# Kernel tuning notes

Measured on AMD Instinct MI355X. Metric: run time of the kernel, lower is better.

The kernel has to match this reference:

```python
import jax, jax.numpy as jnp
import numpy as np

B, S, H, I, E, K = 1, 2048, 1024, 512, 16, 4


def setup_inputs() -> dict:
    key = jax.random.key(0)
    k0, k1, k2, k3, k4, k5 = jax.random.split(key, 6)
    hidden_states = jax.random.normal(k0, (B, S, H), jnp.float32)
    T = B * S
    topk_idx = jax.random.randint(k1, (T, K), 0, E, dtype=jnp.int32)
    raw = jax.random.uniform(k2, (T, K), jnp.float32)
    topk_weight = raw / jnp.sum(raw, axis=-1, keepdims=True)  # normalized top-k gate weights
    scale = 0.02
    w_gate = jax.random.normal(k3, (E, H, I), jnp.float32) * scale
    w_up = jax.random.normal(k4, (E, H, I), jnp.float32) * scale
    w_down = jax.random.normal(k5, (E, I, H), jnp.float32) * scale
    return {
        "hidden_states": hidden_states,
        "topk_idx": topk_idx,
        "topk_weight": topk_weight,
        "w_gate": w_gate,
        "w_up": w_up,
        "w_down": w_down,
    }


def reference(hidden_states, topk_idx, topk_weight, w_gate, w_up, w_down):
    # hidden_states: [B,S,H]; topk_idx/topk_weight: [T,K]; w_*: [E,H,I]/[E,I,H]
    b, s, h = hidden_states.shape
    t = b * s
    e = w_gate.shape[0]
    x = hidden_states.reshape(t, h)
    # routing_weights.scatter_(1, topk_idx, topk_weight)
    routing_weights = jnp.zeros((t, e), x.dtype).at[
        jnp.arange(t)[:, None], topk_idx
    ].set(topk_weight)
    # per-expert gated MLP over all tokens (math identical to masked dispatch:
    # tokens with routing weight 0 contribute nothing)
    g = jnp.einsum("th,ehi->eti", x, w_gate)  # [E,T,I]
    u = jnp.einsum("th,ehi->eti", x, w_up)
    d = jnp.einsum("eti,eih->eth", jax.nn.silu(g) * u, w_down)  # [E,T,H]
    out = jnp.einsum("eth,te->th", d, routing_weights)  # weighted combine
    return out.reshape(b, s, h)
```

## Files before the change

### kernel.cpp

```cpp
#include <hip/hip_runtime.h>
#include <hip/hip_bf16.h>
#include <stdint.h>

#define HH 1024
#define II 512
#define EE 16
#define TT 2048
#define KTOP 4
#define PP (TT * KTOP)
#define MAXROWS 12288

typedef unsigned short u16;
typedef unsigned int u32;
typedef __attribute__((ext_vector_type(8))) short short8;
typedef __attribute__((ext_vector_type(4))) float f32x4;
typedef __attribute__((ext_vector_type(4))) unsigned short u16x4;
typedef __attribute__((ext_vector_type(8))) unsigned short u16x8;
typedef __attribute__((ext_vector_type(4))) unsigned int u32x4;

__device__ __forceinline__ u16 f2bf(float f) {
  union { float f; unsigned u; } v; v.f = f;
  unsigned r = v.u + 0x7fffu + ((v.u >> 16) & 1u);
  return (u16)(r >> 16);
}
__device__ __forceinline__ float bf2f(u16 b) {
  union { unsigned u; float f; } v; v.u = ((unsigned)b) << 16; return v.f;
}

__device__ __forceinline__ void gld16(const u16* g, u16* l) {
  __builtin_amdgcn_global_load_lds(
      (const __attribute__((address_space(1))) unsigned int*)g,
      (__attribute__((address_space(3))) unsigned int*)l, 16, 0, 0);
}

union PLds {
  int s_e[PP];
  u32 t32[128][68];
};

__global__ __launch_bounds__(1024) void prep_fused(
    const float* __restrict__ x, const int* __restrict__ tidx,
    const float* __restrict__ tw,
    const float* __restrict__ wg, const float* __restrict__ wu,
    const float* __restrict__ wd,
    u16* __restrict__ xb, u16* __restrict__ WgT, u16* __restrict__ WuT,
    u16* __restrict__ WdT,
    int* __restrict__ perm, float* __restrict__ wt, int* __restrict__ rowof,
    int* __restrict__ tile_e, int* __restrict__ tile_r,
    int* __restrict__ ntiles) {
  __shared__ PLds L;
  __shared__ int whist[16][16];
  __shared__ int wbase[16][16];
  __shared__ int pad_lo[EE], pad_hi[EE];

  const int bid = blockIdx.x;
  const int tid = threadIdx.x;

  if (bid == 0) {
    const int lane = tid & 63;
    const int wv = tid >> 6;

#pragma unroll
    for (int i = 0; i < 2; i++) {
      const int t = tid + i * 1024;
      const int4 v = ((const int4*)tidx)[t];
      const bool v0 = (v.x != v.y) && (v.x != v.z) && (v.x != v.w);
      const bool v1 = (v.y != v.z) && (v.y != v.w);
      const bool v2 = (v.z != v.w);
      L.s_e[t * 4 + 0] = v.x | (v0 ? 16 : 0);
      L.s_e[t * 4 + 1] = v.y | (v1 ? 16 : 0);
      L.s_e[t * 4 + 2] = v.z | (v2 ? 16 : 0);
      L.s_e[t * 4 + 3] = v.w | 16;
    }
    __syncthreads();

    int h0, h1, h2, h3, h4, h5, h6, h7, h8, h9, h10, h11, h12, h13, h14, h15;
    h0=h1=h2=h3=h4=h5=h6=h7=h8=h9=h10=h11=h12=h13=h14=h15=0;
    const unsigned long long ltm = (1ull << lane) - 1ull;
    for (int c = 0; c < 8; c++) {
      const int p = (wv << 9) + (c << 6) + lane;
      const int se = L.s_e[p];
      const int e = se & 15;
      const bool valid = (se & 16) != 0;
      int rank = 0;
#define RANK_STEP(J, HJ)                                            \
      {                                                             \
        unsigned long long m = __ballot(valid && (e == J));         \
        if (valid && (e == J)) rank = HJ + __popcll(m & ltm);       \
        HJ += __popcll(m);                                          \
      }
      RANK_STEP(0, h0)  RANK_STEP(1, h1)  RANK_STEP(2, h2)  RANK_STEP(3, h3)
      RANK_STEP(4, h4)  RANK_STEP(5, h5)  RANK_STEP(6, h6)  RANK_STEP(7, h7)
      RANK_STEP(8, h8)  RANK_STEP(9, h9)  RANK_STEP(10, h10) RANK_STEP(11, h11)
      RANK_STEP(12, h12) RANK_STEP(13, h13) RANK_STEP(14, h14) RANK_STEP(15, h15)
#undef RANK_STEP
      if (valid) L.s_e[p] = se | (rank << 16);
    }
    if (lane == 0) {
      whist[wv][0] = h0;   whist[wv][1] = h1;   whist[wv][2] = h2;   whist[wv][3] = h3;
      whist[wv][4] = h4;   whist[wv][5] = h5;   whist[wv][6] = h6;   whist[wv][7] = h7;
      whist[wv][8] = h8;   whist[wv][9] = h9;   whist[wv][10] = h10; whist[wv][11] = h11;
      whist[wv][12] = h12; whist[wv][13] = h13; whist[wv][14] = h14; whist[wv][15] = h15;
    }
    __syncthreads();

    if (tid == 0) {
      int off = 0, nt = 0;
      for (int j = 0; j < EE; j++) {
        int tot = 0;
        for (int w = 0; w < 16; w++) { wbase[w][j] = off + tot; tot += whist[w][j]; }
        const int cap = (tot + 127) & ~127;
        pad_lo[j] = off + tot;
        pad_hi[j] = off + cap;
        for (int m0 = 0; m0 < cap; m0 += 128) { tile_e[nt] = j; tile_r[nt] = off + m0; nt++; }
        off += cap;
      }
      *ntiles = nt;
    }
    __syncthreads();

#pragma unroll
    for (int i = 0; i < 8; i++) {
      const int p = i * 1024 + tid;
      const int se = L.s_e[p];
      int pos = -1;
      if (se & 16) {
        const int e = se & 15;
        const int r = se >> 16;
        pos = wbase[p >> 9][e] + r;
        perm[pos] = p >> 2;
        wt[pos] = tw[p];
      }
      rowof[p] = pos;
    }
    for (int j = 0; j < EE; j++) {
      const int lo = pad_lo[j], hi = pad_hi[j];
      for (int i = lo + tid; i < hi; i += 1024) {
        perm[i] = 0;
        wt[i] = 0.f;
      }
    }
    return;
  }

  if (bid <= 128) {
    const int base = ((bid - 1) * 1024 + tid) * 16;
    f32x4 v0 = *(const f32x4*)(x + base);
    f32x4 v1 = *(const f32x4*)(x + base + 4);
    f32x4 v2 = *(const f32x4*)(x + base + 8);
    f32x4 v3 = *(const f32x4*)(x + base + 12);
    u16x8 o0 = { f2bf(v0[0]), f2bf(v0[1]), f2bf(v0[2]), f2bf(v0[3]),
                 f2bf(v1[0]), f2bf(v1[1]), f2bf(v1[2]), f2bf(v1[3]) };
    u16x8 o1 = { f2bf(v2[0]), f2bf(v2[1]), f2bf(v2[2]), f2bf(v2[3]),
                 f2bf(v3[0]), f2bf(v3[1]), f2bf(v3[2]), f2bf(v3[3]) };
    *(u16x8*)(xb + base) = o0;
    *(u16x8*)(xb + base + 8) = o1;
    return;
  }

  const int pb = bid - 129;
  const int matsel = pb >> 9;
  const int within = pb & 511;
  const int zz = within >> 5;
  const int sub = within & 31;
  const float* src; u16* dst; int R, C, xi, yi;
  if (matsel == 0)      { src = wg; dst = WgT; R = HH; C = II; xi = sub & 3; yi = sub >> 2; }
  else if (matsel == 1) { src = wu; dst = WuT; R = HH; C = II; xi = sub & 3; yi = sub >> 2; }
  else                  { src = wd; dst = WdT; R = II; C = HH; xi = sub & 7; yi = sub >> 3; }
  const size_t mat = (size_t)zz * R * C;
  const int r0 = yi * 128, c0 = xi * 128;

  const int rp = tid >> 4, cq8 = (tid & 15) * 8;
  const float* sp = src + mat + (size_t)(r0 + 2 * rp) * C + c0 + cq8;
  const f32x4 a0 = *(const f32x4*)(sp);
  const f32x4 a1 = *(const f32x4*)(sp + 4);
  const f32x4 b0 = *(const f32x4*)(sp + C);
  const f32x4 b1 = *(const f32x4*)(sp + C + 4);

#pragma unroll
  for (int j = 0; j < 4; j++)
    L.t32[cq8 + j][rp] = (u32)f2bf(a0[j]) | ((u32)f2bf(b0[j]) << 16);
#pragma unroll
  for (int j = 0; j < 4; j++)
    L.t32[cq8 + 4 + j][rp] = (u32)f2bf(a1[j]) | ((u32)f2bf(b1[j]) << 16);
  __syncthreads();

  const int c = tid >> 3, q = tid & 7;
  u32x4 v0, v1;
#pragma unroll
  for (int j = 0; j < 4; j++) v0[j] = L.t32[c][q * 8 + j];
#pragma unroll
  for (int j = 0; j < 4; j++) v1[j] = L.t32[c][q * 8 + 4 + j];
  u16* dp = dst + mat + (size_t)(c0 + c) * R + r0 + q * 16;
  *(u32x4*)(dp) = v0;
  *(u32x4*)(dp + 8) = v1;
}

__global__ __launch_bounds__(256) void gemm1_kernel(
    const u16* __restrict__ xb, const u16* __restrict__ WgT, const u16* __restrict__ WuT,
    const int* __restrict__ perm, const float* __restrict__ wt,
    const int* __restrict__ tile_e, const int* __restrict__ tile_r,
    const int* __restrict__ ntiles, u16* __restrict__ ACT) {
  const int tileid = blockIdx.y;
  if (tileid >= *ntiles) return;
  const int e = tile_e[tileid];
  const int row0 = tile_r[tileid];
  const int n0 = blockIdx.x * 64;

  __shared__ __align__(16) u16 As[128 * 64];
  __shared__ __align__(16) u16 Gs[64 * 64];
  __shared__ __align__(16) u16 Us[64 * 64];

  const int tid = threadIdx.x;
  const int lane = tid & 63;
  const int wid = tid >> 6;
  const int wm = wid >> 1, wn = wid & 1;
  const int fr = lane & 15, fq = lane >> 4;

  const int lrow = lane >> 3;
  const int sc8 = ((lane & 7) ^ lrow) * 8;

  const u16* gA[4]; u16* lA[4];
#pragma unroll
  for (int j = 0; j < 4; j++) {
    const int trow = j * 32 + wid * 8 + lrow;
    gA[j] = xb + (size_t)perm[row0 + trow] * HH + sc8;
    lA[j] = As + (j * 4 + wid) * 512;
  }
  const u16 *gG[2], *gU[2];
  u16 *lG[2], *lU[2];
#pragma unroll
  for (int j = 0; j < 2; j++) {
    const int nrow = j * 32 + wid * 8 + lrow;
    gG[j] = WgT + ((size_t)e * II + n0 + nrow) * HH + sc8;
    gU[j] = WuT + ((size_t)e * II + n0 + nrow) * HH + sc8;
    lG[j] = Gs + (j * 4 + wid) * 512;
    lU[j] = Us + (j * 4 + wid) * 512;
  }

  f32x4 accg[4][2], accu[4][2];
  const f32x4 vz = {0.f, 0.f, 0.f, 0.f};
#pragma unroll
  for (int m = 0; m < 4; m++)
#pragma unroll
    for (int n = 0; n < 2; n++) { accg[m][n] = vz; accu[m][n] = vz; }

  for (int k0 = 0; k0 < HH; k0 += 64) {
    __syncthreads();
#pragma unroll
    for (int j = 0; j < 4; j++) gld16(gA[j] + k0, lA[j]);
#pragma unroll
    for (int j = 0; j < 2; j++) { gld16(gG[j] + k0, lG[j]); gld16(gU[j] + k0, lU[j]); }
    __syncthreads();

#pragma unroll
    for (int ks = 0; ks < 2; ks++) {
      short8 af[4], bg[2], bu[2];
#pragma unroll
      for (int m = 0; m < 4; m++) {
        const int r = wm * 64 + m * 16 + fr;
        af[m] = *(const short8*)(&As[r * 64 + (((ks * 4 + fq) ^ (r & 7)) * 8)]);
      }
#pragma unroll
      for (int n = 0; n < 2; n++) {
        const int r = wn * 32 + n * 16 + fr;
        bg[n] = *(const short8*)(&Gs[r * 64 + (((ks * 4 + fq) ^ (r & 7)) * 8)]);
        bu[n] = *(const short8*)(&Us[r * 64 + (((ks * 4 + fq) ^ (r & 7)) * 8)]);
      }
#pragma unroll
      for (int m = 0; m < 4; m++)
#pragma unroll
        for (int n = 0; n < 2; n++) {
          accg[m][n] = __builtin_amdgcn_mfma_f32_16x16x32_bf16(af[m], bg[n], accg[m][n], 0, 0, 0);
          accu[m][n] = __builtin_amdgcn_mfma_f32_16x16x32_bf16(af[m], bu[n], accu[m][n], 0, 0, 0);
        }
    }
  }

#pragma unroll
  for (int m = 0; m < 4; m++) {
    const int rbase = wm * 64 + m * 16 + fq * 4;
#pragma unroll
    for (int j = 0; j < 4; j++) {
      const int rloc = rbase + j;
      const float w = wt[row0 + rloc];
#pragma unroll
      for (int n = 0; n < 2; n++) {
        const float g = accg[m][n][j];
        const float u = accu[m][n][j];
        const float s = g / (1.f + __expf(-g));
        ACT[(size_t)(row0 + rloc) * II + n0 + (wn * 32 + n * 16 + fr)] = f2bf(s * u * w);
      }
    }
  }
}

__global__ __launch_bounds__(256) void gemm2_kernel(
    const u16* __restrict__ ACT, const u16* __restrict__ WdT,
    const int* __restrict__ tile_e, const int* __restrict__ tile_r,
    const int* __restrict__ ntiles, u16* __restrict__ D) {
  const int tileid = blockIdx.y;
  if (tileid >= *ntiles) return;
  const int e = tile_e[tileid];
  const int row0 = tile_r[tileid];
  const int n0 = blockIdx.x * 128;

  __shared__ __align__(16) u16 As[128 * 64];
  __shared__ __align__(16) u16 Bs[128 * 64];

  const int tid = threadIdx.x;
  const int lane = tid & 63;
  const int wid = tid >> 6;
  const int wm = wid >> 1, wn = wid & 1;
  const int fr = lane & 15, fq = lane >> 4;

  const int lrow = lane >> 3;
  const int sc8 = ((lane & 7) ^ lrow) * 8;

  const u16 *gA[4], *gB[4];
  u16 *lA[4], *lB[4];
#pragma unroll
  for (int j = 0; j < 4; j++) {
    const int trow = j * 32 + wid * 8 + lrow;
    gA[j] = ACT + (size_t)(row0 + trow) * II + sc8;
    gB[j] = WdT + ((size_t)e * HH + n0 + trow) * II + sc8;
    lA[j] = As + (j * 4 + wid) * 512;
    lB[j] = Bs + (j * 4 + wid) * 512;
  }

  f32x4 acc[4][4];
  const f32x4 vz = {0.f, 0.f, 0.f, 0.f};
#pragma unroll
  for (int m = 0; m < 4; m++)
#pragma unroll
    for (int n = 0; n < 4; n++) acc[m][n] = vz;

  for (int k0 = 0; k0 < II; k0 += 64) {
    __syncthreads();
#pragma unroll
    for (int j = 0; j < 4; j++) { gld16(gA[j] + k0, lA[j]); gld16(gB[j] + k0, lB[j]); }
    __syncthreads();

#pragma unroll
    for (int ks = 0; ks < 2; ks++) {
      short8 af[4], bf[4];
#pragma unroll
      for (int m = 0; m < 4; m++) {
        const int r = wm * 64 + m * 16 + fr;
        af[m] = *(const short8*)(&As[r * 64 + (((ks * 4 + fq) ^ (r & 7)) * 8)]);
      }
#pragma unroll
      for (int n = 0; n < 4; n++) {
        const int r = wn * 64 + n * 16 + fr;
        bf[n] = *(const short8*)(&Bs[r * 64 + (((ks * 4 + fq) ^ (r & 7)) * 8)]);
      }
#pragma unroll
      for (int m = 0; m < 4; m++)
#pragma unroll
        for (int n = 0; n < 4; n++)
          acc[m][n] = __builtin_amdgcn_mfma_f32_16x16x32_bf16(af[m], bf[n], acc[m][n], 0, 0, 0);
    }
  }

#pragma unroll
  for (int m = 0; m < 4; m++) {
    const int rbase = wm * 64 + m * 16 + fq * 4;
#pragma unroll
    for (int j = 0; j < 4; j++) {
      u16* dp = D + (size_t)(row0 + rbase + j) * HH + n0 + wn * 64 + fr;
#pragma unroll
      for (int n = 0; n < 4; n++)
        dp[n * 16] = f2bf(acc[m][n][j]);
    }
  }
}

__global__ __launch_bounds__(256) void combine_kernel(
    const u16* __restrict__ D, const int* __restrict__ rowof,
    float* __restrict__ out) {
  const int t = blockIdx.x;
  const int h = threadIdx.x * 4;
  const int4 r4 = ((const int4*)rowof)[t];
  float a0 = 0.f, a1 = 0.f, a2 = 0.f, a3 = 0.f;
#define ACCUM(R)                                                     \
  if ((R) >= 0) {                                                    \
    u16x4 d = *(const u16x4*)(D + (size_t)(R) * HH + h);             \
    a0 += bf2f(d[0]); a1 += bf2f(d[1]); a2 += bf2f(d[2]); a3 += bf2f(d[3]); \
  }
  ACCUM(r4.x) ACCUM(r4.y) ACCUM(r4.z) ACCUM(r4.w)
#undef ACCUM
  float4 o = { a0, a1, a2, a3 };
  *(float4*)(out + (size_t)t * HH + h) = o;
}

extern "C" void kernel_launch(void* const* d_in, const int* in_sizes, int n_in,
                              void* d_out, int out_size, void* d_ws, size_t ws_size,
                              hipStream_t stream) {
  const float* x = (const float*)d_in[0];
  const int* tidx = (const int*)d_in[1];
  const float* tw = (const float*)d_in[2];
  const float* wg = (const float*)d_in[3];
  const float* wu = (const float*)d_in[4];
  const float* wd = (const float*)d_in[5];
  float* out = (float*)d_out;

  char* ws = (char*)d_ws;
  int* ntiles = (int*)(ws + 0);
  int* tile_e = (int*)(ws + 1024);
  int* tile_r = (int*)(ws + 2048);
  int* perm = (int*)(ws + 4096);
  float* wt = (float*)(ws + 53248);
  int* rowof = (int*)(ws + 102400);
  u16* xb = (u16*)(ws + 262144);
  u16* WgT = (u16*)(ws + 4456448);
  u16* WuT = (u16*)(ws + 21233664);
  u16* WdT = (u16*)(ws + 38010880);
  u16* ACT = (u16*)(ws + 54788096);
  u16* D = (u16*)(ws + 4456448);

  prep_fused<<<1665, 1024, 0, stream>>>(x, tidx, tw, wg, wu, wd,
                                        xb, WgT, WuT, WdT,
                                        perm, wt, rowof, tile_e, tile_r, ntiles);
  gemm1_kernel<<<dim3(II / 64, 80), 256, 0, stream>>>(xb, WgT, WuT, perm, wt,
                                                      tile_e, tile_r, ntiles, ACT);
  gemm2_kernel<<<dim3(HH / 128, 80), 256, 0, stream>>>(ACT, WdT,
                                                       tile_e, tile_r, ntiles, D);
  combine_kernel<<<TT, 256, 0, stream>>>(D, rowof, out);
}
```

Measured before the change: 81.08 us.

## Split weight transpose blocks into four 256-thread teams with swizzled LDS tiles

The weight transpose/convert section of the prep kernel now gives each 1024-thread block four independent 256-thread teams. Each team transposes a 128x64 tile and has its own LDS slice with an XOR swizzle on the row index. Each thread issues eight float4 loads up front and writes in two passes, which cuts the grid from 1665 to 897 blocks. The aim is fewer LDS bank conflicts and more memory-level parallelism per thread. The cost is more registers and more complicated indexing, and a wrong swizzle would silently corrupt the transposed weights.

```diff
diff --git a/kernel.cpp b/kernel.cpp
--- a/kernel.cpp
+++ b/kernel.cpp
@@ -26,6 +26,9 @@
 __device__ __forceinline__ float bf2f(u16 b) {
   union { unsigned u; float f; } v; v.u = ((unsigned)b) << 16; return v.f;
 }
+__device__ __forceinline__ u32 packbf(float lo, float hi) {
+  return (u32)f2bf(lo) | ((u32)f2bf(hi) << 16);
+}
 
 __device__ __forceinline__ void gld16(const u16* g, u16* l) {
   __builtin_amdgcn_global_load_lds(
@@ -35,7 +38,7 @@
 
 union PLds {
   int s_e[PP];
-  u32 t32[128][68];
+  u32 t4[4][64][68];
 };
 
 __global__ __launch_bounds__(1024) void prep_fused(
@@ -158,42 +161,65 @@
     return;
   }
 
-  const int pb = bid - 129;
-  const int matsel = pb >> 9;
-  const int within = pb & 511;
-  const int zz = within >> 5;
-  const int sub = within & 31;
-  const float* src; u16* dst; int R, C, xi, yi;
-  if (matsel == 0)      { src = wg; dst = WgT; R = HH; C = II; xi = sub & 3; yi = sub >> 2; }
-  else if (matsel == 1) { src = wu; dst = WuT; R = HH; C = II; xi = sub & 3; yi = sub >> 2; }
-  else                  { src = wd; dst = WdT; R = II; C = HH; xi = sub & 7; yi = sub >> 3; }
-  const size_t mat = (size_t)zz * R * C;
-  const int r0 = yi * 128, c0 = xi * 128;
-
-  const int rp = tid >> 4, cq8 = (tid & 15) * 8;
-  const float* sp = src + mat + (size_t)(r0 + 2 * rp) * C + c0 + cq8;
-  const f32x4 a0 = *(const f32x4*)(sp);
-  const f32x4 a1 = *(const f32x4*)(sp + 4);
-  const f32x4 b0 = *(const f32x4*)(sp + C);
-  const f32x4 b1 = *(const f32x4*)(sp + C + 4);
-
-#pragma unroll
-  for (int j = 0; j < 4; j++)
-    L.t32[cq8 + j][rp] = (u32)f2bf(a0[j]) | ((u32)f2bf(b0[j]) << 16);
-#pragma unroll
-  for (int j = 0; j < 4; j++)
-    L.t32[cq8 + 4 + j][rp] = (u32)f2bf(a1[j]) | ((u32)f2bf(b1[j]) << 16);
+  const int team = tid >> 8;
+  const int t = tid & 255;
+  const int g = (bid - 129) * 4 + team;
+  const int matsel = g >> 10;
+  const int w = g & 1023;
+  const int zz = w >> 6;
+  const int sub = w & 63;
+  const float* src; u16* dst; int C, Rout, r0, c0;
+  if (matsel == 0)      { src = wg; dst = WgT; C = II; Rout = HH; r0 = (sub >> 3) * 128; c0 = (sub & 7) * 64; }
+  else if (matsel == 1) { src = wu; dst = WuT; C = II; Rout = HH; r0 = (sub >> 3) * 128; c0 = (sub & 7) * 64; }
+  else                  { src = wd; dst = WdT; C = HH; Rout = II; r0 = (sub >> 4) * 128; c0 = (sub & 15) * 64; }
+  const size_t mat = (size_t)zz * HH * II;
+  u32 (*T32)[68] = L.t4[team];
+
+  const int rpA = t >> 3;
+  const int cq8 = (t & 7) * 8;
+  const float* spA = src + mat + (size_t)(r0 + 2 * rpA) * C + c0 + cq8;
+  const float* spB = spA + (size_t)64 * C;
+  const f32x4 a0 = *(const f32x4*)(spA);
+  const f32x4 a1 = *(const f32x4*)(spA + 4);
+  const f32x4 b0 = *(const f32x4*)(spA + C);
+  const f32x4 b1 = *(const f32x4*)(spA + C + 4);
+  const f32x4 e0 = *(const f32x4*)(spB);
+  const f32x4 e1 = *(const f32x4*)(spB + 4);
+  const f32x4 g0 = *(const f32x4*)(spB + HH * 0 + C);
+  const f32x4 g1 = *(const f32x4*)(spB + C + 4);
+  __builtin_amdgcn_sched_barrier(0);
+
+  const int key = t & 7;
+  const int sw = ((key & 7) << 3) ^ (((key >> 2) & 1) << 2);
+  const int rpxA = rpA ^ sw;
+  const int rpxB = (rpA + 32) ^ sw;
+#pragma unroll
+  for (int j = 0; j < 4; j++) T32[cq8 + j][rpxA] = packbf(a0[j], b0[j]);
+#pragma unroll
+  for (int j = 0; j < 4; j++) T32[cq8 + 4 + j][rpxA] = packbf(a1[j], b1[j]);
+#pragma unroll
+  for (int j = 0; j < 4; j++) T32[cq8 + j][rpxB] = packbf(e0[j], g0[j]);
+#pragma unroll
+  for (int j = 0; j < 4; j++) T32[cq8 + 4 + j][rpxB] = packbf(e1[j], g1[j]);
   __syncthreads();
 
-  const int c = tid >> 3, q = tid & 7;
-  u32x4 v0, v1;
-#pragma unroll
-  for (int j = 0; j < 4; j++) v0[j] = L.t32[c][q * 8 + j];
-#pragma unroll
-  for (int j = 0; j < 4; j++) v1[j] = L.t32[c][q * 8 + 4 + j];
-  u16* dp = dst + mat + (size_t)(c0 + c) * R + r0 + q * 16;
-  *(u32x4*)(dp) = v0;
-  *(u32x4*)(dp + 8) = v1;
+  const int c = t >> 2;
+  const int q2 = t & 3;
+  const int rkey = c >> 3;
+  const int b2 = ((rkey >> 2) & 1) * 4;
+#pragma unroll
+  for (int pass = 0; pass < 2; pass++) {
+    const int o = q2 + pass * 4;
+    const int qb = (o ^ (rkey & 7)) * 8;
+    u32x4 v0, v1;
+#pragma unroll
+    for (int j = 0; j < 4; j++) v0[j] = T32[c][qb + b2 + j];
+#pragma unroll
+    for (int j = 0; j < 4; j++) v1[j] = T32[c][qb + (b2 ^ 4) + j];
+    u16* dp = dst + mat + (size_t)(c0 + c) * Rout + r0 + o * 16;
+    *(u32x4*)(dp) = v0;
+    *(u32x4*)(dp + 8) = v1;
+  }
 }
 
 __global__ __launch_bounds__(256) void gemm1_kernel(
@@ -418,9 +444,9 @@
   u16* ACT = (u16*)(ws + 54788096);
   u16* D = (u16*)(ws + 4456448);
 
-  prep_fused<<<1665, 1024, 0, stream>>>(x, tidx, tw, wg, wu, wd,
-                                        xb, WgT, WuT, WdT,
-                                        perm, wt, rowof, tile_e, tile_r, ntiles);
+  prep_fused<<<897, 1024, 0, stream>>>(x, tidx, tw, wg, wu, wd,
+                                       xb, WgT, WuT, WdT,
+                                       perm, wt, rowof, tile_e, tile_r, ntiles);
   gemm1_kernel<<<dim3(II / 64, 80), 256, 0, stream>>>(xb, WgT, WuT, perm, wt,
                                                       tile_e, tile_r, ntiles, ACT);
   gemm2_kernel<<<dim3(HH / 128, 80), 256, 0, stream>>>(ACT, WdT,
```

Result: faster. 78.98 us (-2.6%).
